# Kernel optimization log

Hardware: AMD Instinct MI355X
Metric: run time of the kernel (lower is better)

Reference implementation:

```python
import jax, jax.numpy as jnp
import numpy as np

EMBED_DIM = 64
NUM_HEADS = 8
D_K = EMBED_DIM // NUM_HEADS  # n_wires = 8, state dim 2**8 = 256


def _rx_gate(theta):
    # theta: scalar or [N]; returns [..., 2, 2] complex64
    c = jnp.cos(theta / 2).astype(jnp.complex64)
    s = (-1j) * jnp.sin(theta / 2).astype(jnp.complex64)
    return jnp.stack([jnp.stack([c, s], -1), jnp.stack([s, c], -1)], -2)


def _rz_gate(theta):
    e0 = jnp.exp(-1j * theta.astype(jnp.complex64) / 2)
    e1 = jnp.exp(1j * theta.astype(jnp.complex64) / 2)
    z = jnp.zeros_like(e0)
    return jnp.stack([jnp.stack([e0, z], -1), jnp.stack([z, e1], -1)], -2)


def _apply_1q(state, gate, wire):
    # state: [N] + [2]*n ; gate [2,2] (shared) or [N,2,2] (per-token)
    s = jnp.moveaxis(state, 1 + wire, 1)
    if gate.ndim == 2:
        s = jnp.einsum('ab,nb...->na...', gate, s)
    else:
        s = jnp.einsum('nab,nb...->na...', gate, s)
    return jnp.moveaxis(s, 1, 1 + wire)


def _apply_cnot(state, ctrl, tgt):
    s0 = jax.lax.index_in_dim(state, 0, axis=1 + ctrl, keepdims=True)
    s1 = jax.lax.index_in_dim(state, 1, axis=1 + ctrl, keepdims=True)
    s1 = jnp.flip(s1, axis=1 + tgt)
    return jnp.concatenate([s0, s1], axis=1 + ctrl)


def _pauli_z_signs(n):
    idx = np.arange(2 ** n)
    bits = (idx[None, :] >> (n - 1 - np.arange(n)[:, None])) & 1  # [n, 2**n]
    return jnp.asarray(1.0 - 2.0 * bits, dtype=jnp.float32)


def _qlayer(tokens, params_rx, params_rz):
    # tokens: [N, n] float32 -> PauliZ expectations [N, n]
    N, n = tokens.shape
    depth = params_rx.shape[0]
    state = jnp.zeros((N,) + (2,) * n, dtype=jnp.complex64)
    state = state.at[(slice(None),) + (0,) * n].set(1.0)
    # data-encoding RX per wire (per-token angle)
    for w in range(n):
        state = _apply_1q(state, _rx_gate(tokens[:, w]), w)
    for l in range(depth):
        for w in range(n):
            state = _apply_1q(state, _rx_gate(params_rx[l, w]), w)
            state = _apply_1q(state, _rz_gate(params_rz[l, w]), w)
        for w in range(n - 1):
            state = _apply_cnot(state, w, w + 1)
        state = _apply_cnot(state, n - 1, 0)
    probs = jnp.abs(state.reshape(N, -1)) ** 2  # [N, 2**n]
    signs = _pauli_z_signs(n)  # [n, 2**n]
    return probs @ signs.T  # [N, n]


def setup_inputs() -> dict:
    key = jax.random.key(0)
    k1, k2, k3, k4 = jax.random.split(key, 4)
    B, S = 4, 512
    depth = 2
    return {
        'x': jax.random.normal(k1, (B, S, EMBED_DIM), dtype=jnp.float32),
        'params_rx': jax.random.normal(k2, (depth, D_K), dtype=jnp.float32),
        'params_rz': jax.random.normal(k3, (depth, D_K), dtype=jnp.float32),
        'W_combine': jax.random.normal(k4, (EMBED_DIM, EMBED_DIM), dtype=jnp.float32) * 0.05,
    }


def reference(x, params_rx, params_rz, W_combine):
    B, S, E = x.shape
    H, dk = NUM_HEADS, D_K
    # separate_heads: [B,S,E] -> [B,H,S,dk], then flatten all tokens
    xh = x.reshape(B, S, H, dk).transpose(0, 2, 1, 3)
    tokens = xh.reshape(B * H * S, dk)
    out = _qlayer(tokens, params_rx, params_rz)  # [N, dk]
    out = out.reshape(B, H, S, dk).transpose(0, 2, 1, 3).reshape(B, S, E)
    return out @ W_combine.T
```

## Files before the change

kernel.cpp:

```cpp
#include <hip/hip_runtime.h>


struct C2 { float re, im; };
__device__ __forceinline__ C2 cmul(C2 a, C2 b){ return {a.re*b.re - a.im*b.im, a.re*b.im + a.im*b.re}; }
__device__ __forceinline__ C2 cadd(C2 a, C2 b){ return {a.re+b.re, a.im+b.im}; }
__device__ __forceinline__ C2 csc (C2 a, float k){ return {a.re*k, a.im*k}; }

__host__ __device__ constexpr int phmul(int a, int b) {
    if (a == 0 || b == 0 || a == b) return 0;
    if ((a == 1 && b == 2) || (a == 2 && b == 3) || (a == 3 && b == 1)) return 1;
    return 3;
}

template<int A, int B, int Cc, int D>
__device__ __forceinline__ C2 pexp(const float* m) {
    constexpr int p1 = phmul(A, B);          constexpr int c1 = A ^ B;
    constexpr int p2 = p1 + phmul(c1, Cc);   constexpr int c2 = c1 ^ Cc;
    constexpr int p3 = p2 + phmul(c2, D);    constexpr int c3 = c2 ^ D;
    constexpr int ph = p3 & 3;
    float v = m[c3];
    C2 r{0.f, 0.f};
    if constexpr (ph == 0) r.re = v;
    else if constexpr (ph == 1) r.im = v;
    else if constexpr (ph == 2) r.re = -v;
    else r.im = -v;
    return r;
}

template<int LEAD, int WT, int R, int RMAX>
__device__ __forceinline__ void mid(C2& gz, C2& gy, const float (*m)[4],
                                    const float* kc, const float* ks) {
    if constexpr (R <= RMAX) {
        constexpr int TZ = ((WT - R) & 1) ? 3 : 0;
        C2 hz = cadd(cmul(gz, pexp<LEAD,0,3,TZ>(m[R])), cmul(gy, pexp<LEAD,1,3,TZ>(m[R])));
        C2 hy = cadd(cmul(gz, pexp<LEAD,0,2,TZ>(m[R])), cmul(gy, pexp<LEAD,1,2,TZ>(m[R])));
        gz = csc(hz, kc[R]); gy = csc(hy, ks[R]);
        mid<LEAD, WT, R + 1, RMAX>(gz, gy, m, kc, ks);
    }
}

template<int W>
__device__ __forceinline__ float chainW(const float (*m)[4], const float* kc,
                                        const float* ks, const float* SZ) {
    constexpr int T0 = (W & 1) ? 3 : 0;
    C2 gz = csc(pexp<0,T0,0,0>(m[0]), kc[0]);
    C2 gy = csc(pexp<1,T0,0,0>(m[0]), ks[0]);
    constexpr int T1 = ((W - 1) & 1) ? 3 : 0;
    C2 hz = cadd(cmul(gz, pexp<3,3,T1,0>(m[1])), cmul(gy, pexp<2,3,T1,0>(m[1])));
    C2 hy = cadd(cmul(gz, pexp<3,2,T1,0>(m[1])), cmul(gy, pexp<2,2,T1,0>(m[1])));
    gz = csc(hz, kc[1]); gy = csc(hy, ks[1]);
    mid<3, W, 2, W>(gz, gy, m, kc, ks);
    C2 t = cadd(cmul(gz, pexp<3,0,0,0>(m[W+1])), cmul(gy, pexp<3,1,0,0>(m[W+1])));
    return t.re * SZ[W + 2];
}

__device__ __forceinline__ float chain7(const float (*m)[4], const float* kc,
                                        const float* ks) {
    float out;
    {
        C2 gz = csc(pexp<0,3,0,0>(m[0]), kc[0]);
        C2 gy = csc(pexp<1,3,0,0>(m[0]), ks[0]);
        C2 hz = cadd(cmul(gz, pexp<3,3,0,0>(m[1])), cmul(gy, pexp<2,3,0,0>(m[1])));
        C2 hy = cadd(cmul(gz, pexp<3,2,0,0>(m[1])), cmul(gy, pexp<2,2,0,0>(m[1])));
        gz = csc(hz, kc[1]); gy = csc(hy, ks[1]);
        mid<3, 7, 2, 6>(gz, gy, m, kc, ks);
        C2 t = cadd(cmul(gz, pexp<3,0,3,0>(m[7])), cmul(gy, pexp<3,1,3,0>(m[7])));
        out = t.re * kc[7];
    }
    {
        C2 gz = csc(pexp<0,2,0,0>(m[0]), kc[0]);
        C2 gy = csc(pexp<1,2,0,0>(m[0]), ks[0]);
        C2 hz = cadd(cmul(gz, pexp<3,3,3,2>(m[1])), cmul(gy, pexp<2,3,3,2>(m[1])));
        C2 hy = cadd(cmul(gz, pexp<3,2,3,2>(m[1])), cmul(gy, pexp<2,2,3,2>(m[1])));
        gz = csc(hz, kc[1]); gy = csc(hy, ks[1]);
        mid<3, 7, 2, 6>(gz, gy, m, kc, ks);
        C2 t = cadd(cmul(gz, pexp<3,0,2,0>(m[7])), cmul(gy, pexp<3,1,2,0>(m[7])));
        out -= t.re * ks[7];
    }
    return out;
}

__device__ __forceinline__ float chain0(const float (*m)[4], const float* kc,
                                        const float* ks) {
    float out;
    {
        C2 gz = csc(pexp<3,0,0,0>(m[1]), kc[1] * m[0][3]);
        C2 gy = csc(pexp<2,0,0,0>(m[1]), ks[1] * m[0][3]);
        mid<0, 7, 2, 6>(gz, gy, m, kc, ks);
        C2 t = cadd(cmul(gz, pexp<0,3,0,0>(m[7])), cmul(gy, pexp<1,3,0,0>(m[7])));
        out = t.re * kc[7];
    }
    {
        C2 gz = csc(pexp<3,3,2,0>(m[1]), kc[1] * m[0][2]);
        C2 gy = csc(pexp<2,3,2,0>(m[1]), ks[1] * m[0][2]);
        mid<0, 7, 2, 6>(gz, gy, m, kc, ks);
        C2 t = cadd(cmul(gz, pexp<0,2,0,0>(m[7])), cmul(gy, pexp<1,2,0,0>(m[7])));
        out -= t.re * ks[7];
    }
    return out;
}

__global__ __launch_bounds__(64)
void MultiHeadAttentionQuantum_65481071396433_kernel(
        const float* __restrict__ x,
        const float* __restrict__ prx,
        const float* __restrict__ prz,
        const float* __restrict__ W,
        float* __restrict__ out,
        int depth)
{
    __shared__ float cf[40];
    __shared__ float qs[8][64];
    const int tid = threadIdx.x;

    if (tid < 8) {
        int w = tid;
        float sp, cp;
        __sincosf(prz[w], &sp, &cp);
        cf[w] = cp; cf[8 + w] = sp;
        cf[16 + w] = prx[w];
        float s1, c1;
        __sincosf(prx[(depth - 1) * 8 + w], &s1, &c1);
        cf[24 + w] = c1; cf[32 + w] = s1;
    }
    __syncthreads();

    const int t = blockIdx.x * 64 + tid;
    const float4* xp = (const float4*)(x + t * 8);
    float4 xa = xp[0], xb = xp[1];
    float th[8] = {xa.x, xa.y, xa.z, xa.w, xb.x, xb.y, xb.z, xb.w};

    float m[8][4];
    float kc[8], ks[8];
#pragma unroll
    for (int w = 0; w < 8; ++w) {
        float st, ct;
        __sincosf(th[w] + cf[16 + w], &st, &ct);
        m[w][0] = 1.f;
        m[w][1] = st * cf[8 + w];
        m[w][2] = -st * cf[w];
        m[w][3] = ct;
        kc[w] = cf[24 + w]; ks[w] = cf[32 + w];
    }
    float SZ[9];
    SZ[8] = 1.f;
#pragma unroll
    for (int r = 7; r >= 3; --r) SZ[r] = SZ[r + 1] * m[r][3];

    float q[8];
    q[0] = chain0(m, kc, ks);
    q[1] = chainW<1>(m, kc, ks, SZ);
    q[2] = chainW<2>(m, kc, ks, SZ);
    q[3] = chainW<3>(m, kc, ks, SZ);
    q[4] = chainW<4>(m, kc, ks, SZ);
    q[5] = chainW<5>(m, kc, ks, SZ);
    q[6] = chainW<6>(m, kc, ks, SZ);
    q[7] = chain7(m, kc, ks);

    const int rl = tid >> 3, h = tid & 7;
#pragma unroll
    for (int w = 0; w < 8; ++w) qs[rl][h * 8 + w] = q[w];
    __syncthreads();

    const int e = tid;
    const float4* Wr = (const float4*)(W + e * 64);
    float4 wreg[16];
#pragma unroll
    for (int j = 0; j < 16; ++j) wreg[j] = Wr[j];
    const int row0 = blockIdx.x * 8;
#pragma unroll
    for (int r = 0; r < 8; ++r) {
        const float4* qr = (const float4*)qs[r];
        float acc = 0.f;
#pragma unroll
        for (int j = 0; j < 16; ++j) {
            float4 qv = qr[j];
            float4 wv = wreg[j];
            acc = fmaf(qv.x, wv.x, acc);
            acc = fmaf(qv.y, wv.y, acc);
            acc = fmaf(qv.z, wv.z, acc);
            acc = fmaf(qv.w, wv.w, acc);
        }
        out[(row0 + r) * 64 + e] = acc;
    }
}

extern "C" void kernel_launch(void* const* d_in, const int* in_sizes, int n_in,
                              void* d_out, int out_size, void* d_ws, size_t ws_size,
                              hipStream_t stream) {
    const float* x   = (const float*)d_in[0];
    const float* prx = (const float*)d_in[1];
    const float* prz = (const float*)d_in[2];
    const float* W   = (const float*)d_in[3];
    float* out = (float*)d_out;

    int depth  = in_sizes[1] / 8;
    int tokens = in_sizes[0] / 8;
    int blocks = tokens / 64;

    MultiHeadAttentionQuantum_65481071396433_kernel<<<blocks, 64, 0, stream>>>(
        x, prx, prz, W, out, depth);
}
```

Measured before the change: 62.90 us.

## Share transfer-matrix prefix chains across PauliZ outputs of same parity

Replaces the independent per-wire chain computations with shared running chains. Odd wires (1,3,5,7) reuse one forward chain, even wires (2,4,6) reuse another, and each output is read off at an intermediate step with a cheap closing expression. This removes redundant complex multiply steps that the earlier code recomputed for every output wire. Correctness depends on the parity-based TZ pattern matching the original chains exactly.

Result: no change. 62.69 us (-0.3%).

```diff
diff --git a/kernel.cpp b/kernel.cpp
--- a/kernel.cpp
+++ b/kernel.cpp
@@ -27,77 +27,24 @@
     return r;
 }
 
-template<int LEAD, int WT, int R, int RMAX>
-__device__ __forceinline__ void mid(C2& gz, C2& gy, const float (*m)[4],
-                                    const float* kc, const float* ks) {
-    if constexpr (R <= RMAX) {
-        constexpr int TZ = ((WT - R) & 1) ? 3 : 0;
-        C2 hz = cadd(cmul(gz, pexp<LEAD,0,3,TZ>(m[R])), cmul(gy, pexp<LEAD,1,3,TZ>(m[R])));
-        C2 hy = cadd(cmul(gz, pexp<LEAD,0,2,TZ>(m[R])), cmul(gy, pexp<LEAD,1,2,TZ>(m[R])));
-        gz = csc(hz, kc[R]); gy = csc(hy, ks[R]);
-        mid<LEAD, WT, R + 1, RMAX>(gz, gy, m, kc, ks);
-    }
+struct V2 { C2 gz, gy; };
+
+template<int LEAD, int TZ>
+__device__ __forceinline__ void mstep(V2& v, const float* mr, float kcr, float ksr) {
+    C2 hz = cadd(cmul(v.gz, pexp<LEAD,0,3,TZ>(mr)), cmul(v.gy, pexp<LEAD,1,3,TZ>(mr)));
+    C2 hy = cadd(cmul(v.gz, pexp<LEAD,0,2,TZ>(mr)), cmul(v.gy, pexp<LEAD,1,2,TZ>(mr)));
+    v.gz = csc(hz, kcr); v.gy = csc(hy, ksr);
 }
 
-template<int W>
-__device__ __forceinline__ float chainW(const float (*m)[4], const float* kc,
-                                        const float* ks, const float* SZ) {
-    constexpr int T0 = (W & 1) ? 3 : 0;
-    C2 gz = csc(pexp<0,T0,0,0>(m[0]), kc[0]);
-    C2 gy = csc(pexp<1,T0,0,0>(m[0]), ks[0]);
-    constexpr int T1 = ((W - 1) & 1) ? 3 : 0;
-    C2 hz = cadd(cmul(gz, pexp<3,3,T1,0>(m[1])), cmul(gy, pexp<2,3,T1,0>(m[1])));
-    C2 hy = cadd(cmul(gz, pexp<3,2,T1,0>(m[1])), cmul(gy, pexp<2,2,T1,0>(m[1])));
-    gz = csc(hz, kc[1]); gy = csc(hy, ks[1]);
-    mid<3, W, 2, W>(gz, gy, m, kc, ks);
-    C2 t = cadd(cmul(gz, pexp<3,0,0,0>(m[W+1])), cmul(gy, pexp<3,1,0,0>(m[W+1])));
-    return t.re * SZ[W + 2];
+__device__ __forceinline__ float closeO(const V2& v, const float* mn, float szv) {
+    return (v.gz.re * mn[3] - v.gy.im * mn[2]) * szv;
 }
 
-__device__ __forceinline__ float chain7(const float (*m)[4], const float* kc,
-                                        const float* ks) {
-    float out;
-    {
-        C2 gz = csc(pexp<0,3,0,0>(m[0]), kc[0]);
-        C2 gy = csc(pexp<1,3,0,0>(m[0]), ks[0]);
-        C2 hz = cadd(cmul(gz, pexp<3,3,0,0>(m[1])), cmul(gy, pexp<2,3,0,0>(m[1])));
-        C2 hy = cadd(cmul(gz, pexp<3,2,0,0>(m[1])), cmul(gy, pexp<2,2,0,0>(m[1])));
-        gz = csc(hz, kc[1]); gy = csc(hy, ks[1]);
-        mid<3, 7, 2, 6>(gz, gy, m, kc, ks);
-        C2 t = cadd(cmul(gz, pexp<3,0,3,0>(m[7])), cmul(gy, pexp<3,1,3,0>(m[7])));
-        out = t.re * kc[7];
-    }
-    {
-        C2 gz = csc(pexp<0,2,0,0>(m[0]), kc[0]);
-        C2 gy = csc(pexp<1,2,0,0>(m[0]), ks[0]);
-        C2 hz = cadd(cmul(gz, pexp<3,3,3,2>(m[1])), cmul(gy, pexp<2,3,3,2>(m[1])));
-        C2 hy = cadd(cmul(gz, pexp<3,2,3,2>(m[1])), cmul(gy, pexp<2,2,3,2>(m[1])));
-        gz = csc(hz, kc[1]); gy = csc(hy, ks[1]);
-        mid<3, 7, 2, 6>(gz, gy, m, kc, ks);
-        C2 t = cadd(cmul(gz, pexp<3,0,2,0>(m[7])), cmul(gy, pexp<3,1,2,0>(m[7])));
-        out -= t.re * ks[7];
-    }
-    return out;
-}
-
-__device__ __forceinline__ float chain0(const float (*m)[4], const float* kc,
-                                        const float* ks) {
-    float out;
-    {
-        C2 gz = csc(pexp<3,0,0,0>(m[1]), kc[1] * m[0][3]);
-        C2 gy = csc(pexp<2,0,0,0>(m[1]), ks[1] * m[0][3]);
-        mid<0, 7, 2, 6>(gz, gy, m, kc, ks);
-        C2 t = cadd(cmul(gz, pexp<0,3,0,0>(m[7])), cmul(gy, pexp<1,3,0,0>(m[7])));
-        out = t.re * kc[7];
-    }
-    {
-        C2 gz = csc(pexp<3,3,2,0>(m[1]), kc[1] * m[0][2]);
-        C2 gy = csc(pexp<2,3,2,0>(m[1]), ks[1] * m[0][2]);
-        mid<0, 7, 2, 6>(gz, gy, m, kc, ks);
-        C2 t = cadd(cmul(gz, pexp<0,2,0,0>(m[7])), cmul(gy, pexp<1,2,0,0>(m[7])));
-        out -= t.re * ks[7];
-    }
-    return out;
+template<int Bz, int By, int Cc, int D>
+__device__ __forceinline__ void w1step(V2& v, const float* m1, float kc1, float ks1) {
+    C2 hz = cadd(cmul(v.gz, pexp<3,Bz,Cc,D>(m1)), cmul(v.gy, pexp<2,Bz,Cc,D>(m1)));
+    C2 hy = cadd(cmul(v.gz, pexp<3,By,Cc,D>(m1)), cmul(v.gy, pexp<2,By,Cc,D>(m1)));
+    v.gz = csc(hz, kc1); v.gy = csc(hy, ks1);
 }
 
 __global__ __launch_bounds__(64)
@@ -148,14 +95,60 @@
     for (int r = 7; r >= 3; --r) SZ[r] = SZ[r + 1] * m[r][3];
 
     float q[8];
-    q[0] = chain0(m, kc, ks);
-    q[1] = chainW<1>(m, kc, ks, SZ);
-    q[2] = chainW<2>(m, kc, ks, SZ);
-    q[3] = chainW<3>(m, kc, ks, SZ);
-    q[4] = chainW<4>(m, kc, ks, SZ);
-    q[5] = chainW<5>(m, kc, ks, SZ);
-    q[6] = chainW<6>(m, kc, ks, SZ);
-    q[7] = chain7(m, kc, ks);
+
+    {
+        V2 F;
+        F.gz = csc(pexp<0,3,0,0>(m[0]), kc[0]);
+        F.gy = csc(pexp<1,3,0,0>(m[0]), ks[0]);
+        w1step<3,2,0,0>(F, m[1], kc[1], ks[1]);
+        V2 R;
+        R.gz = csc(pexp<0,2,0,0>(m[0]), kc[0]);
+        R.gy = csc(pexp<1,2,0,0>(m[0]), ks[0]);
+        w1step<3,2,3,2>(R, m[1], kc[1], ks[1]);
+
+        q[1] = closeO(F, m[2], SZ[3]);
+        mstep<3,3>(F, m[2], kc[2], ks[2]);  mstep<3,3>(R, m[2], kc[2], ks[2]);
+        mstep<3,0>(F, m[3], kc[3], ks[3]);  mstep<3,0>(R, m[3], kc[3], ks[3]);
+        q[3] = closeO(F, m[4], SZ[5]);
+        mstep<3,3>(F, m[4], kc[4], ks[4]);  mstep<3,3>(R, m[4], kc[4], ks[4]);
+        mstep<3,0>(F, m[5], kc[5], ks[5]);  mstep<3,0>(R, m[5], kc[5], ks[5]);
+        q[5] = closeO(F, m[6], SZ[7]);
+        mstep<3,3>(F, m[6], kc[6], ks[6]);  mstep<3,3>(R, m[6], kc[6], ks[6]);
+        float tz = F.gz.re - F.gy.re * m[7][1];
+        float ty = R.gz.im * m[7][1] - R.gy.im;
+        q[7] = tz * kc[7] - ty * ks[7];
+    }
+
+    {
+        V2 E;
+        E.gz = csc(pexp<0,0,0,0>(m[0]), kc[0]);
+        E.gy = csc(pexp<1,0,0,0>(m[0]), ks[0]);
+        w1step<3,2,3,0>(E, m[1], kc[1], ks[1]);
+        mstep<3,0>(E, m[2], kc[2], ks[2]);
+        q[2] = closeO(E, m[3], SZ[4]);
+        mstep<3,3>(E, m[3], kc[3], ks[3]);
+        mstep<3,0>(E, m[4], kc[4], ks[4]);
+        q[4] = closeO(E, m[5], SZ[6]);
+        mstep<3,3>(E, m[5], kc[5], ks[5]);
+        mstep<3,0>(E, m[6], kc[6], ks[6]);
+        q[6] = closeO(E, m[7], SZ[8]);
+    }
+
+    {
+        V2 Zc, Yc;
+        Zc.gz = csc(pexp<3,0,0,0>(m[1]), kc[1] * m[0][3]);
+        Zc.gy = csc(pexp<2,0,0,0>(m[1]), ks[1] * m[0][3]);
+        Yc.gz = csc(pexp<3,3,2,0>(m[1]), kc[1] * m[0][2]);
+        Yc.gy = csc(pexp<2,3,2,0>(m[1]), ks[1] * m[0][2]);
+        mstep<0,3>(Zc, m[2], kc[2], ks[2]);  mstep<0,3>(Yc, m[2], kc[2], ks[2]);
+        mstep<0,0>(Zc, m[3], kc[3], ks[3]);  mstep<0,0>(Yc, m[3], kc[3], ks[3]);
+        mstep<0,3>(Zc, m[4], kc[4], ks[4]);  mstep<0,3>(Yc, m[4], kc[4], ks[4]);
+        mstep<0,0>(Zc, m[5], kc[5], ks[5]);  mstep<0,0>(Yc, m[5], kc[5], ks[5]);
+        mstep<0,3>(Zc, m[6], kc[6], ks[6]);  mstep<0,3>(Yc, m[6], kc[6], ks[6]);
+        float tz = Zc.gz.re * m[7][3] + Zc.gy.im * m[7][2];
+        float ty = Yc.gz.re * m[7][2] - Yc.gy.im * m[7][3];
+        q[0] = tz * kc[7] - ty * ks[7];
+    }
 
     const int rl = tid >> 3, h = tid & 7;
 #pragma unroll
```
